# Performance work log

Measured on AMD Instinct MI355X. Metric: run time of the kernel, lower is better.

Reference implementation:

```python
import jax, jax.numpy as jnp
import numpy as np

KERNEL = 3  # kernel_size from init_kwargs


def _unfold(x, k):
    """torch.nn.functional.unfold with padding=k//2, stride=1.
    Returns [b, c*k*k, h*w] with torch's ordering: index = c*(k*k) + kh*k + kw.
    """
    b, c, h, w = x.shape
    p = k // 2
    xp = jnp.pad(x, ((0, 0), (0, 0), (p, p), (p, p)))
    # fixed k*k = 9 slices (small static loop, not a data-dim loop)
    cols = jnp.stack(
        [xp[:, :, i:i + h, j:j + w] for i in range(k) for j in range(k)],
        axis=2,
    )  # [b, c, k*k, h, w]
    return cols.reshape(b, c * k * k, h * w)


def setup_inputs() -> dict:
    key = jax.random.key(0)
    k1, k2 = jax.random.split(key)
    x = jax.random.normal(k1, (8, 64, 128, 128), dtype=jnp.float32)
    # memory parameter: torch.rand -> uniform [0, 1), shape [c*k*k, out_channels]
    memory = jax.random.uniform(k2, (64 * KERNEL * KERNEL, 128), dtype=jnp.float32)
    return {"x": x, "memory": memory}


def reference(x, memory):
    b, c, h, w = x.shape
    cols = _unfold(x, KERNEL)                 # [b, c*k*k, h*w]
    cols = jax.nn.softmax(cols, axis=1)       # softmax over unfolded patch dim
    out = jnp.einsum('ki,bkl->bil', memory, cols)  # [b, out_ch, h*w]
    return out.reshape(b, memory.shape[1], h, w)
```

## Files before the change

### kernel.cpp

```cpp
#include <hip/hip_runtime.h>
#include <stdint.h>


#define Cn 64
#define Hn 128
#define Wn 128
#define OC 128
#define HW (Hn * Wn)

typedef __attribute__((ext_vector_type(8))) short bf16x8_t;
typedef __attribute__((ext_vector_type(16))) float f32x16_t;

__device__ inline unsigned short f2bf(float f) {
    union { float f; uint32_t u; } v; v.f = f;
    uint32_t u = v.u;
    u += 0x7fffu + ((u >> 16) & 1u);
    return (unsigned short)(u >> 16);
}
__device__ inline float bf_lo(uint32_t u) {
    union { uint32_t u; float f; } v; v.u = u << 16;
    return v.f;
}
__device__ inline float bf_hi(uint32_t u) {
    union { uint32_t u; float f; } v; v.u = u & 0xffff0000u;
    return v.f;
}

__global__ void prep_b2(const float* __restrict__ mem, uint4* __restrict__ Bt2) {
    int u = blockIdx.x * 256 + threadIdx.x;
    int n = u & 127;
    int cid = u >> 7;
    int hi = cid & 1;
    int kc = cid >> 1;
    int q = kc >> 2, cblk = kc & 3;
    unsigned short h8[8];
#pragma unroll
    for (int j = 0; j < 8; j++) {
        int c = cblk * 16 + hi * 8 + j;
        h8[j] = f2bf(mem[(c * 9 + q) * OC + n]);
    }
    Bt2[cid * 128 + n] = *(const uint4*)h8;
}

__global__ __launch_bounds__(512, 4) void convf(const float* __restrict__ x,
                                                const uint4* __restrict__ Bt2,
                                                float* __restrict__ out) {
    __shared__ __align__(16) uint4 EtL[180 * 8];
    __shared__ float Sh[180];
    __shared__ float Zt[128];

    int bid0 = blockIdx.x;
    int bid = ((bid0 & 7) << 7) | (bid0 >> 3);
    int b = bid >> 7;
    int ty = (bid >> 3) & 15, tx = bid & 7;
    int h0 = ty * 8, w0 = tx * 16;
    int t = threadIdx.x;

    const float* xb = x + (size_t)b * Cn * HW;
    const uint4 PAD = make_uint4(0x3F803F80u, 0x3F803F80u, 0x3F803F80u, 0x3F803F80u);

    if (t < 480) {
        int qs = t % 6;
        int v6 = t / 6;
        int py = v6 % 10;
        int g  = v6 / 10;
        int gy = h0 - 1 + py;
        bool inrow = (gy >= 0) & (gy < Hn);
        int xg = w0 - 4 + qs * 4;
        const float* base = xb + (size_t)(8 * g) * HW + (size_t)gy * Wn + xg;

        if (qs >= 1 && qs <= 4) {
            if (inrow) {
                float4 v[8];
#pragma unroll
                for (int k = 0; k < 8; k++)
                    v[k] = *(const float4*)(base + (size_t)k * HW);
#pragma unroll
                for (int i = 0; i < 4; i++) {
                    uint32_t wd[4];
#pragma unroll
                    for (int j = 0; j < 4; j++) {
                        float a = ((const float*)&v[2 * j])[i];
                        float c = ((const float*)&v[2 * j + 1])[i];
                        wd[j] = (uint32_t)f2bf(__expf(a)) | ((uint32_t)f2bf(__expf(c)) << 16);
                    }
                    int p = py * 18 + (qs - 1) * 4 + 1 + i;
                    EtL[p * 8 + (g ^ ((p >> 1) & 7))] = *(const uint4*)wd;
                }
            } else {
#pragma unroll
                for (int i = 0; i < 4; i++) {
                    int p = py * 18 + (qs - 1) * 4 + 1 + i;
                    EtL[p * 8 + (g ^ ((p >> 1) & 7))] = PAD;
                }
            }
        } else {
            int side = (qs == 5);
            int p = py * 18 + (side ? 17 : 0);
            bool real = inrow && (side ? (tx < 7) : (tx > 0));
            uint4 gran = PAD;
            if (real) {
                float4 v[8];
#pragma unroll
                for (int k = 0; k < 8; k++)
                    v[k] = *(const float4*)(base + (size_t)k * HW);
                uint32_t wd[4];
#pragma unroll
                for (int j = 0; j < 4; j++) {
                    float a = side ? ((const float*)&v[2 * j])[0]     : ((const float*)&v[2 * j])[3];
                    float c = side ? ((const float*)&v[2 * j + 1])[0] : ((const float*)&v[2 * j + 1])[3];
                    wd[j] = (uint32_t)f2bf(__expf(a)) | ((uint32_t)f2bf(__expf(c)) << 16);
                }
                gran = *(const uint4*)wd;
            }
            EtL[p * 8 + (g ^ ((p >> 1) & 7))] = gran;
        }
    }
    __syncthreads();

    if (t < 180) {
        float s = 0.f;
#pragma unroll
        for (int k = 0; k < 8; k++) {
            uint4 q = EtL[t * 8 + ((k + t) & 7)];
            s += bf_lo(q.x) + bf_hi(q.x) + bf_lo(q.y) + bf_hi(q.y)
               + bf_lo(q.z) + bf_hi(q.z) + bf_lo(q.w) + bf_hi(q.w);
        }
        Sh[t] = s;
    }
    __syncthreads();

    if (t < 128) {
        int zy = t >> 4, zx = t & 15;
        float z = 0.f;
#pragma unroll
        for (int dy = 0; dy < 3; dy++)
#pragma unroll
            for (int dx = 0; dx < 3; dx++)
                z += Sh[(zy + dy) * 18 + (zx + dx)];
        Zt[t] = 1.0f / z;
    }
    __syncthreads();

    int lane = t & 63;
    int wid = t >> 6;
    int wo = wid & 3;
    int wp = wid >> 2;
    int l31 = lane & 31, hi = lane >> 5;
    int x0v = l31 & 15;
    int y0[2];
    y0[0] = (wp * 2 + 0) * 2 + (l31 >> 4);
    y0[1] = (wp * 2 + 1) * 2 + (l31 >> 4);

    f32x16_t acc[2];
#pragma unroll
    for (int j = 0; j < 2; j++)
#pragma unroll
        for (int r = 0; r < 16; r++) acc[j][r] = 0.f;

    bf16x8_t Wf[3], Ef[3][2];

    auto loadW = [&](int kc, int s) {
        Wf[s] = *(const bf16x8_t*)(Bt2 + (size_t)((kc * 2 + hi) * 128 + wo * 32 + l31));
    };
    auto loadE = [&](int kc, int s) {
        int q = kc >> 2, cblk = kc & 3;
        int kh = q / 3, kw = q - kh * 3;
        int ge = cblk * 2 + hi;
#pragma unroll
        for (int j = 0; j < 2; j++) {
            int pix = (y0[j] + kh) * 18 + (x0v + kw);
            Ef[s][j] = *(const bf16x8_t*)&EtL[pix * 8 + (ge ^ ((pix >> 1) & 7))];
        }
    };

    loadW(0, 0); loadE(0, 0);
    loadW(1, 1); loadE(1, 1);
    loadW(2, 2); loadE(2, 2);
#pragma unroll
    for (int kc = 0; kc < 36; kc++) {
        int s = kc % 3;
#pragma unroll
        for (int j = 0; j < 2; j++)
            acc[j] = __builtin_amdgcn_mfma_f32_32x32x16_bf16(
                Wf[s], Ef[s][j], acc[j], 0, 0, 0);
        if (kc + 3 < 36) { loadW(kc + 3, s); loadE(kc + 3, s); }
    }

#pragma unroll
    for (int j = 0; j < 2; j++) {
        float zi = Zt[(y0[j] << 4) | x0v];
        float* ob = out + (size_t)b * OC * HW + (size_t)(wo * 32 + 4 * hi) * HW
                  + (h0 + y0[j]) * Wn + (w0 + x0v);
#pragma unroll
        for (int r = 0; r < 16; r++) {
            int nrel = (r & 3) + 8 * (r >> 2);
            ob[(size_t)nrel * HW] = acc[j][r] * zi;
        }
    }
}

extern "C" void kernel_launch(void* const* d_in, const int* in_sizes, int n_in,
                              void* d_out, int out_size, void* d_ws, size_t ws_size,
                              hipStream_t stream) {
    const float* x = (const float*)d_in[0];
    const float* mem = (const float*)d_in[1];
    float* out = (float*)d_out;

    uint4* Bt2 = (uint4*)d_ws;

    prep_b2<<<36, 256, 0, stream>>>(mem, Bt2);
    convf<<<1024, 512, 0, stream>>>(x, Bt2, out);
}
```

Before: 112.4 us.

## Halve spatial tile to 4x16 with 256 threads and fuse softmax sums via shuffles

```diff
diff --git a/kernel.cpp b/kernel.cpp
--- a/kernel.cpp
+++ b/kernel.cpp
@@ -42,115 +42,113 @@
     Bt2[cid * 128 + n] = *(const uint4*)h8;
 }
 
-__global__ __launch_bounds__(512, 4) void convf(const float* __restrict__ x,
+__global__ __launch_bounds__(256, 4) void convf(const float* __restrict__ x,
                                                 const uint4* __restrict__ Bt2,
                                                 float* __restrict__ out) {
-    __shared__ __align__(16) uint4 EtL[180 * 8];
-    __shared__ float Sh[180];
-    __shared__ float Zt[128];
+    __shared__ __align__(16) uint4 EtL[108 * 8];
+    __shared__ float Sh[108];
 
     int bid0 = blockIdx.x;
-    int bid = ((bid0 & 7) << 7) | (bid0 >> 3);
-    int b = bid >> 7;
-    int ty = (bid >> 3) & 15, tx = bid & 7;
-    int h0 = ty * 8, w0 = tx * 16;
+    int bid = ((bid0 & 7) << 8) | (bid0 >> 3);
+    int b = bid >> 8;
+    int ty = (bid >> 3) & 31, tx = bid & 7;
+    int h0 = ty * 4, w0 = tx * 16;
     int t = threadIdx.x;
+    int lane = t & 63;
 
     const float* xb = x + (size_t)b * Cn * HW;
-    const uint4 PAD = make_uint4(0x3F803F80u, 0x3F803F80u, 0x3F803F80u, 0x3F803F80u);
-
-    if (t < 480) {
-        int qs = t % 6;
-        int v6 = t / 6;
-        int py = v6 % 10;
-        int g  = v6 / 10;
-        int gy = h0 - 1 + py;
-        bool inrow = (gy >= 0) & (gy < Hn);
-        int xg = w0 - 4 + qs * 4;
-        const float* base = xb + (size_t)(8 * g) * HW + (size_t)gy * Wn + xg;
-
-        if (qs >= 1 && qs <= 4) {
-            if (inrow) {
+
+#pragma unroll
+    for (int it = 0; it < 2; it++) {
+        int u = it * 256 + t;
+        if (u < 288) {
+            int g = u & 7;
+            int pg = u >> 3;
+            int py = pg / 6, qs = pg % 6;
+            int gy = h0 - 1 + py;
+            bool inrow = (gy >= 0) & (gy < Hn);
+
+            if (qs >= 1 && qs <= 4) {
+                int px0 = (qs - 1) * 4 + 1;
                 float4 v[8];
-#pragma unroll
-                for (int k = 0; k < 8; k++)
-                    v[k] = *(const float4*)(base + (size_t)k * HW);
+                if (inrow) {
+                    const float* basep = xb + (size_t)(8 * g) * HW
+                                       + (size_t)gy * Wn + (w0 + (qs - 1) * 4);
+#pragma unroll
+                    for (int k = 0; k < 8; k++)
+                        v[k] = *(const float4*)(basep + (size_t)k * HW);
+                }
+                float s4[4];
 #pragma unroll
                 for (int i = 0; i < 4; i++) {
                     uint32_t wd[4];
+                    float si;
+                    if (inrow) {
+                        si = 0.f;
+#pragma unroll
+                        for (int j = 0; j < 4; j++) {
+                            float a = ((const float*)&v[2 * j])[i];
+                            float c = ((const float*)&v[2 * j + 1])[i];
+                            uint32_t pk = (uint32_t)f2bf(__expf(a))
+                                        | ((uint32_t)f2bf(__expf(c)) << 16);
+                            wd[j] = pk;
+                            si += bf_lo(pk) + bf_hi(pk);
+                        }
+                    } else {
+                        wd[0] = wd[1] = wd[2] = wd[3] = 0x3F803F80u;
+                        si = 8.f;
+                    }
+                    int p = py * 18 + px0 + i;
+                    EtL[p * 8 + (g ^ (p & 7))] = *(const uint4*)wd;
+                    s4[i] = si;
+                }
+#pragma unroll
+                for (int m = 1; m < 8; m <<= 1) {
+#pragma unroll
+                    for (int i = 0; i < 4; i++)
+                        s4[i] += __shfl_xor(s4[i], m);
+                }
+                if (g < 4) Sh[py * 18 + px0 + g] = s4[g];
+            } else {
+                int side = (qs == 5);
+                int p = py * 18 + (side ? 17 : 0);
+                int gxe = side ? (w0 + 16) : (w0 - 1);
+                bool real = inrow && (gxe >= 0) && (gxe < Wn);
+                uint32_t wd[4];
+                float s;
+                if (real) {
+                    const float* basep = xb + (size_t)(8 * g) * HW
+                                       + (size_t)gy * Wn + gxe;
+                    s = 0.f;
 #pragma unroll
                     for (int j = 0; j < 4; j++) {
-                        float a = ((const float*)&v[2 * j])[i];
-                        float c = ((const float*)&v[2 * j + 1])[i];
-                        wd[j] = (uint32_t)f2bf(__expf(a)) | ((uint32_t)f2bf(__expf(c)) << 16);
+                        float a = basep[(size_t)(2 * j) * HW];
+                        float c = basep[(size_t)(2 * j + 1) * HW];
+                        uint32_t pk = (uint32_t)f2bf(__expf(a))
+                                    | ((uint32_t)f2bf(__expf(c)) << 16);
+                        wd[j] = pk;
+                        s += bf_lo(pk) + bf_hi(pk);
                     }
-                    int p = py * 18 + (qs - 1) * 4 + 1 + i;
-                    EtL[p * 8 + (g ^ ((p >> 1) & 7))] = *(const uint4*)wd;
-                }
-            } else {
-#pragma unroll
-                for (int i = 0; i < 4; i++) {
-                    int p = py * 18 + (qs - 1) * 4 + 1 + i;
-                    EtL[p * 8 + (g ^ ((p >> 1) & 7))] = PAD;
-                }
+                } else {
+                    wd[0] = wd[1] = wd[2] = wd[3] = 0x3F803F80u;
+                    s = 8.f;
+                }
+                EtL[p * 8 + (g ^ (p & 7))] = *(const uint4*)wd;
+#pragma unroll
+                for (int m = 1; m < 8; m <<= 1)
+                    s += __shfl_xor(s, m);
+                if (g == 0) Sh[p] = s;
             }
-        } else {
-            int side = (qs == 5);
-            int p = py * 18 + (side ? 17 : 0);
-            bool real = inrow && (side ? (tx < 7) : (tx > 0));
-            uint4 gran = PAD;
-            if (real) {
-                float4 v[8];
-#pragma unroll
-                for (int k = 0; k < 8; k++)
-                    v[k] = *(const float4*)(base + (size_t)k * HW);
-                uint32_t wd[4];
-#pragma unroll
-                for (int j = 0; j < 4; j++) {
-                    float a = side ? ((const float*)&v[2 * j])[0]     : ((const float*)&v[2 * j])[3];
-                    float c = side ? ((const float*)&v[2 * j + 1])[0] : ((const float*)&v[2 * j + 1])[3];
-                    wd[j] = (uint32_t)f2bf(__expf(a)) | ((uint32_t)f2bf(__expf(c)) << 16);
-                }
-                gran = *(const uint4*)wd;
-            }
-            EtL[p * 8 + (g ^ ((p >> 1) & 7))] = gran;
         }
     }
     __syncthreads();
 
-    if (t < 180) {
-        float s = 0.f;
-#pragma unroll
-        for (int k = 0; k < 8; k++) {
-            uint4 q = EtL[t * 8 + ((k + t) & 7)];
-            s += bf_lo(q.x) + bf_hi(q.x) + bf_lo(q.y) + bf_hi(q.y)
-               + bf_lo(q.z) + bf_hi(q.z) + bf_lo(q.w) + bf_hi(q.w);
-        }
-        Sh[t] = s;
-    }
-    __syncthreads();
-
-    if (t < 128) {
-        int zy = t >> 4, zx = t & 15;
-        float z = 0.f;
-#pragma unroll
-        for (int dy = 0; dy < 3; dy++)
-#pragma unroll
-            for (int dx = 0; dx < 3; dx++)
-                z += Sh[(zy + dy) * 18 + (zx + dx)];
-        Zt[t] = 1.0f / z;
-    }
-    __syncthreads();
-
-    int lane = t & 63;
-    int wid = t >> 6;
-    int wo = wid & 3;
-    int wp = wid >> 2;
+    int wo = t >> 6;
     int l31 = lane & 31, hi = lane >> 5;
     int x0v = l31 & 15;
     int y0[2];
-    y0[0] = (wp * 2 + 0) * 2 + (l31 >> 4);
-    y0[1] = (wp * 2 + 1) * 2 + (l31 >> 4);
+    y0[0] = 0 + (l31 >> 4);
+    y0[1] = 2 + (l31 >> 4);
 
     f32x16_t acc[2];
 #pragma unroll
@@ -158,7 +156,7 @@
 #pragma unroll
         for (int r = 0; r < 16; r++) acc[j][r] = 0.f;
 
-    bf16x8_t Wf[3], Ef[3][2];
+    bf16x8_t Wf[4], Ef[4][2];
 
     auto loadW = [&](int kc, int s) {
         Wf[s] = *(const bf16x8_t*)(Bt2 + (size_t)((kc * 2 + hi) * 128 + wo * 32 + l31));
@@ -170,26 +168,33 @@
 #pragma unroll
         for (int j = 0; j < 2; j++) {
             int pix = (y0[j] + kh) * 18 + (x0v + kw);
-            Ef[s][j] = *(const bf16x8_t*)&EtL[pix * 8 + (ge ^ ((pix >> 1) & 7))];
+            Ef[s][j] = *(const bf16x8_t*)&EtL[pix * 8 + (ge ^ (pix & 7))];
         }
     };
 
     loadW(0, 0); loadE(0, 0);
     loadW(1, 1); loadE(1, 1);
     loadW(2, 2); loadE(2, 2);
+    loadW(3, 3); loadE(3, 3);
 #pragma unroll
     for (int kc = 0; kc < 36; kc++) {
-        int s = kc % 3;
+        int s = kc & 3;
 #pragma unroll
         for (int j = 0; j < 2; j++)
             acc[j] = __builtin_amdgcn_mfma_f32_32x32x16_bf16(
                 Wf[s], Ef[s][j], acc[j], 0, 0, 0);
-        if (kc + 3 < 36) { loadW(kc + 3, s); loadE(kc + 3, s); }
+        if (kc + 4 < 36) { loadW(kc + 4, s); loadE(kc + 4, s); }
     }
 
 #pragma unroll
     for (int j = 0; j < 2; j++) {
-        float zi = Zt[(y0[j] << 4) | x0v];
+        float z = 0.f;
+#pragma unroll
+        for (int dy = 0; dy < 3; dy++)
+#pragma unroll
+            for (int dx = 0; dx < 3; dx++)
+                z += Sh[(y0[j] + dy) * 18 + (x0v + dx)];
+        float zi = 1.0f / z;
         float* ob = out + (size_t)b * OC * HW + (size_t)(wo * 32 + 4 * hi) * HW
                   + (h0 + y0[j]) * Wn + (w0 + x0v);
 #pragma unroll
@@ -210,5 +215,5 @@
     uint4* Bt2 = (uint4*)d_ws;
 
     prep_b2<<<36, 256, 0, stream>>>(mem, Bt2);
-    convf<<<1024, 512, 0, stream>>>(x, Bt2, out);
-}
+    convf<<<2048, 256, 0, stream>>>(x, Bt2, out);
+}
```

Measured after the change: 135.4 us. 1.2x slower.
